# Performance work log

Hardware: AMD Instinct MI355X
Metric: run time of the kernel (lower is better)

## Reference

```python
import jax, jax.numpy as jnp
import numpy as np

TEMPERATURE = 12.5   # init temperature
SINKHORN_EPS = 0.05  # entropic regularization replacing exact cv2.EMD LP solve
SINKHORN_ITERS = 100 # fixed iteration count (jit-friendly)


def _weight_vector(A, B):
    # A: [M,C,H,W], B: [N,C,H,W] -> [M, N, H*W]
    # matches: global-avg-pool B over HW, inner product over channels per spatial node of A
    Bp = B.mean(axis=(2, 3))                      # [N, C]
    comb = jnp.einsum('mchw,nc->mnhw', A, Bp)     # [M, N, H, W]
    comb = comb.reshape(A.shape[0], B.shape[0], -1)
    return jax.nn.relu(comb) + 0.001


def _center(x):
    # norm='center': subtract channel mean (dim 1)
    return x - x.mean(axis=1, keepdims=True)


def _similarity_map(support, query):
    # metric='cosine': sim[q, w, i, j] = cos(query[q,:,i], support[w,:,j]) over channels
    s = support.reshape(support.shape[0], support.shape[1], -1)  # [W, C, Ns]
    q = query.reshape(query.shape[0], query.shape[1], -1)        # [Q, C, Nq]
    s = s / jnp.maximum(jnp.linalg.norm(s, axis=1, keepdims=True), 1e-8)
    q = q / jnp.maximum(jnp.linalg.norm(q, axis=1, keepdims=True), 1e-8)
    return jnp.einsum('qci,wcj->qwij', q, s)                     # [Q, W, Nq, Ns]


def _sinkhorn_flow(cost, a, b, eps=SINKHORN_EPS, n_iters=SINKHORN_ITERS):
    # Batched entropic OT in log-space. cost: [..., n, m]; a: [..., n]; b: [..., m].
    log_a = jnp.log(a)
    log_b = jnp.log(b)
    logK = -cost / eps

    def body(_, uv):
        u, v = uv
        u = log_a - jax.nn.logsumexp(logK + v[..., None, :], axis=-1)
        v = log_b - jax.nn.logsumexp(logK + u[..., None], axis=-2)
        return (u, v)

    u0 = jnp.zeros_like(log_a)
    v0 = jnp.zeros_like(log_b)
    u, v = jax.lax.fori_loop(0, n_iters, body, (u0, v0))
    return jnp.exp(logK + u[..., None] + v[..., None, :])  # transport plan [..., n, m]


def setup_inputs() -> dict:
    key = jax.random.key(0)
    k1, k2 = jax.random.split(key)
    support = jax.random.normal(k1, (32, 512, 8, 8), dtype=jnp.float32)
    query = jax.random.normal(k2, (256, 512, 8, 8), dtype=jnp.float32)
    return {"support": support, "query": query}


def reference(support, query):
    # weight_1: [Q, W, N] (row/query-node marginals), weight_2: [W, Q, N] (col/support-node)
    w1 = _weight_vector(query, support)
    w2 = _weight_vector(support, query)

    s = _center(support)
    q = _center(query)
    sim = _similarity_map(s, q)  # [Q, W, N, N]

    num_node = w1.shape[-1]
    # opencv path: relu (no-op, already >0) + 1e-5, rescale so each marginal sums to num_node
    a = w1 + 1e-5
    a = a * (num_node / a.sum(-1, keepdims=True))              # [Q, W, N]
    b = jnp.transpose(w2, (1, 0, 2)) + 1e-5                    # weight_2[j, i] -> [Q, W, N]
    b = b * (num_node / b.sum(-1, keepdims=True))

    flow = _sinkhorn_flow(1.0 - sim, a, b)                     # [Q, W, N, N]
    flow = jax.lax.stop_gradient(flow)  # opencv flow is a non-differentiable constant

    logits = (sim * flow).sum((-1, -2)) * (TEMPERATURE / num_node)  # [Q, W]
    return logits
```

## Files before the change

### kernel.cpp

```cpp
#include <hip/hip_runtime.h>
#include <math.h>


#define DEV static __device__ __forceinline__

typedef _Float16 half8 __attribute__((ext_vector_type(8)));
typedef float floatx4 __attribute__((ext_vector_type(4)));
typedef float floatx2 __attribute__((ext_vector_type(2)));

DEV float fast_rcp(float x) {
#if __has_builtin(__builtin_amdgcn_rcpf)
    return __builtin_amdgcn_rcpf(x);
#else
    return 1.0f / x;
#endif
}
DEV float fexp2(float x) {
#if __has_builtin(__builtin_amdgcn_exp2f)
    return __builtin_amdgcn_exp2f(x);
#else
    return exp2f(x);
#endif
}
DEV float flog2(float x) {
#if __has_builtin(__builtin_amdgcn_logf)
    return __builtin_amdgcn_logf(x);
#else
    return log2f(x);
#endif
}
DEV floatx2 pk_mul(floatx2 a, floatx2 b) {
    floatx2 d;
    asm("v_pk_mul_f32 %0, %1, %2" : "=v"(d) : "v"(a), "v"(b));
    return d;
}
DEV floatx2 pk_fma(floatx2 a, floatx2 b, floatx2 c) {
    floatx2 d;
    asm("v_pk_fma_f32 %0, %1, %2, %3" : "=v"(d) : "v"(a), "v"(b), "v"(c));
    return d;
}

#define K_SIM2M 28.853900817779268f
#define K_M2SIM 0.034657359027997264f
#define LDPH 72

__global__ void __launch_bounds__(1024, 1)
norm_kernel(const float* __restrict__ support, const float* __restrict__ query,
            _Float16* __restrict__ Vht, _Float16* __restrict__ Uht,
            float* __restrict__ muA, float* __restrict__ nrmA,
            float* __restrict__ Ssc) {
    __shared__ float red1[16][64];
    __shared__ float red2[16][64];
    __shared__ float muL[64], invL[64];
    __shared__ float tile[128][65];

    int sid = blockIdx.x;
    const float* src;
    _Float16* dst;
    if (sid < 32) {
        src = support + (size_t)sid * 32768; dst = Vht + (size_t)sid * 32768;
    } else {
        src = query + (size_t)(sid - 32) * 32768; dst = Uht + (size_t)(sid - 32) * 32768;
    }

    int node = threadIdx.x & 63;
    int cq   = threadIdx.x >> 6;

    float s1 = 0.f, s2 = 0.f;
#pragma unroll 8
    for (int j = 0; j < 32; ++j) {
        int c = cq * 32 + j;
        float x = src[c * 64 + node];
        s1 += x; s2 += x * x;
    }
    red1[cq][node] = s1;
    red2[cq][node] = s2;
    __syncthreads();
    if (threadIdx.x < 64) {
        float t1 = 0.f, t2 = 0.f;
#pragma unroll
        for (int k = 0; k < 16; ++k) { t1 += red1[k][node]; t2 += red2[k][node]; }
        float mu  = t1 * (1.0f / 512.0f);
        float ss  = t2 - 512.0f * mu * mu;
        float nrm = fmaxf(sqrtf(fmaxf(ss, 0.0f)), 1e-8f);
        muL[node]  = mu;
        invL[node] = 1.0f / nrm;
        muA[sid * 64 + node]  = mu;
        nrmA[sid * 64 + node] = nrm;
        float sS = t1;
        sS += __shfl_xor(sS, 1);  sS += __shfl_xor(sS, 2);  sS += __shfl_xor(sS, 4);
        sS += __shfl_xor(sS, 8);  sS += __shfl_xor(sS, 16); sS += __shfl_xor(sS, 32);
        if (node == 0) Ssc[sid] = sS * (1.0f / 64.0f);
    }
    __syncthreads();

    float mu = muL[node], inv = invL[node];
    for (int ch = 0; ch < 4; ++ch) {
#pragma unroll
        for (int j = 0; j < 8; ++j) {
            int cl = cq * 8 + j;
            float x = src[(ch * 128 + cl) * 64 + node];
            tile[cl][node] = (x - mu) * inv;
        }
        __syncthreads();
        {
            int g    = threadIdx.x;
            int slot = g & 63;
            int t    = (g >> 6) & 3;
            int kkl  = g >> 8;
            int nd   = t * 16 + (slot & 15);
            int c8   = (kkl << 2) | (slot >> 4);
            half8 v;
#pragma unroll
            for (int i = 0; i < 8; ++i) v[i] = (_Float16)tile[c8 * 8 + i][nd];
            *(half8*)(dst + ((size_t)ch * 1024 + g) * 8) = v;
        }
        __syncthreads();
    }
}

__global__ void __launch_bounds__(256, 4)
emd_kernel(const _Float16* __restrict__ Uht, const _Float16* __restrict__ Vht,
           const float* __restrict__ muA, const float* __restrict__ nrmA,
           const float* __restrict__ Ssc, float* __restrict__ out) {
    __shared__ __align__(16) _Float16 T[4][64 * LDPH];
    __shared__ float dAB[4][128];

    int x    = blockIdx.x & 7;
    int i    = blockIdx.x >> 3;
    int w    = i & 31;
    int wave = threadIdx.x >> 6;
    int lane = threadIdx.x & 63;
    int q    = x * 32 + (i >> 5) * 4 + wave;
    int lo16 = lane & 15;
    int hi4  = lane >> 4;
    int ig   = lane >> 3;
    int jg   = lane & 7;

    floatx4 acc[4][4];
#pragma unroll
    for (int tm = 0; tm < 4; ++tm)
#pragma unroll
        for (int tn = 0; tn < 4; ++tn)
            acc[tm][tn] = (floatx4){0.f, 0.f, 0.f, 0.f};

    const _Float16* Abase = Uht + (size_t)q * 32768 + lane * 8;
    const _Float16* Bbase = Vht + (size_t)w * 32768 + lane * 8;
#pragma unroll 1
    for (int kk = 0; kk < 16; ++kk) {
        half8 bf[4];
#pragma unroll
        for (int t = 0; t < 4; ++t)
            bf[t] = *(const half8*)(Bbase + (size_t)(kk * 4 + t) * 512);
#pragma unroll
        for (int tm = 0; tm < 4; ++tm) {
            half8 af = *(const half8*)(Abase + (size_t)(kk * 4 + tm) * 512);
#pragma unroll
            for (int tn = 0; tn < 4; ++tn)
                acc[tm][tn] = __builtin_amdgcn_mfma_f32_16x16x32_f16(
                    af, bf[tn], acc[tm][tn], 0, 0, 0);
        }
    }

    {
        float nw[4];
#pragma unroll
        for (int tn = 0; tn < 4; ++tn)
            nw[tn] = nrmA[w * 64 + tn * 16 + lo16];
        float4 nq[4];
#pragma unroll
        for (int tm = 0; tm < 4; ++tm)
            nq[tm] = *(const float4*)(nrmA + (32 + q) * 64 + tm * 16 + hi4 * 4);

        float pA[4][4];
#pragma unroll
        for (int tm = 0; tm < 4; ++tm)
#pragma unroll
            for (int r = 0; r < 4; ++r) {
                float s = acc[tm][0][r] * nw[0];
                s = fmaf(acc[tm][1][r], nw[1], s);
                s = fmaf(acc[tm][2][r], nw[2], s);
                s = fmaf(acc[tm][3][r], nw[3], s);
                s += __shfl_xor(s, 1); s += __shfl_xor(s, 2);
                s += __shfl_xor(s, 4); s += __shfl_xor(s, 8);
                pA[tm][r] = s;
            }
        float pB[4];
#pragma unroll
        for (int tn = 0; tn < 4; ++tn) {
            float s = acc[0][tn][0] * nq[0].x;
            s = fmaf(acc[0][tn][1], nq[0].y, s);
            s = fmaf(acc[0][tn][2], nq[0].z, s);
            s = fmaf(acc[0][tn][3], nq[0].w, s);
#pragma unroll
            for (int tm = 1; tm < 4; ++tm) {
                s = fmaf(acc[tm][tn][0], nq[tm].x, s);
                s = fmaf(acc[tm][tn][1], nq[tm].y, s);
                s = fmaf(acc[tm][tn][2], nq[tm].z, s);
                s = fmaf(acc[tm][tn][3], nq[tm].w, s);
            }
            s += __shfl_xor(s, 16); s += __shfl_xor(s, 32);
            pB[tn] = s;
        }
        float* dA = dAB[wave];
        float* dB = dAB[wave] + 64;
        if (lo16 == 0) {
#pragma unroll
            for (int tm = 0; tm < 4; ++tm)
#pragma unroll
                for (int r = 0; r < 4; ++r)
                    dA[tm * 16 + hi4 * 4 + r] = pA[tm][r] * 0.015625f;
        }
        if (hi4 == 0) {
#pragma unroll
            for (int tn = 0; tn < 4; ++tn)
                dB[tn * 16 + lo16] = pB[tn] * 0.015625f;
        }
    }

    float lmax = -2.0f;
#pragma unroll
    for (int tm = 0; tm < 4; ++tm)
#pragma unroll
        for (int tn = 0; tn < 4; ++tn)
#pragma unroll
            for (int r = 0; r < 4; ++r) lmax = fmaxf(lmax, acc[tm][tn][r]);
    lmax = fmaxf(lmax, __shfl_xor(lmax, 1));
    lmax = fmaxf(lmax, __shfl_xor(lmax, 2));
    lmax = fmaxf(lmax, __shfl_xor(lmax, 4));
    lmax = fmaxf(lmax, __shfl_xor(lmax, 8));
    lmax = fmaxf(lmax, __shfl_xor(lmax, 16));
    lmax = fmaxf(lmax, __shfl_xor(lmax, 32));
    float s0 = lmax;

    {
        _Float16* buf = T[wave];
#pragma unroll
        for (int tm = 0; tm < 4; ++tm)
#pragma unroll
            for (int tn = 0; tn < 4; ++tn)
#pragma unroll
                for (int r = 0; r < 4; ++r) {
                    int row = tm * 16 + hi4 * 4 + r;
                    int col = tn * 16 + lo16;
                    int sp  = (col & 7) ^ (row >> 3);
                    buf[row * LDPH + (col & ~7) + sp] =
                        (_Float16)fexp2((acc[tm][tn][r] - s0) * K_SIM2M);
                }
    }
    floatx2 Mp[8][4];
    {
        const _Float16* buf = T[wave];
#pragma unroll
        for (int t = 0; t < 8; ++t) {
            half8 h = *(const half8*)(buf + (ig * 8 + (jg ^ t)) * LDPH + jg * 8);
#pragma unroll
            for (int j = 0; j < 4; ++j)
                Mp[t][j] = (floatx2){(float)h[2 * j], (float)h[2 * j + 1]};
        }
    }

    int gp = q * 32 + w;
    float a_own, b_own;
    {
        const float* dA = dAB[wave];
        const float* dB = dAB[wave] + 64;
        float Sw = Ssc[w];
        float Sq = Ssc[32 + q];
        float muq = muA[(32 + q) * 64 + lane];
        float nrq = nrmA[(32 + q) * 64 + lane];
        float va = fmaxf(fmaf(muq, Sw, nrq * dA[lane]), 0.0f) + 0.001f;
        va += 1e-5f;
        float sa = va;
        sa += __shfl_xor(sa, 1);  sa += __shfl_xor(sa, 2);  sa += __shfl_xor(sa, 4);
        sa += __shfl_xor(sa, 8);  sa += __shfl_xor(sa, 16); sa += __shfl_xor(sa, 32);
        a_own = va * (64.0f / sa);
        int nb = ((lane & 7) << 3) | (lane >> 3);
        float muw = muA[w * 64 + nb];
        float nrw = nrmA[w * 64 + nb];
        float vb = fmaxf(fmaf(muw, Sq, nrw * dB[nb]), 0.0f) + 0.001f;
        vb += 1e-5f;
        float sb = vb;
        sb += __shfl_xor(sb, 1);  sb += __shfl_xor(sb, 2);  sb += __shfl_xor(sb, 4);
        sb += __shfl_xor(sb, 8);  sb += __shfl_xor(sb, 16); sb += __shfl_xor(sb, 32);
        b_own = vb * (64.0f / sb);
    }

    floatx2 wv2[4];
#pragma unroll
    for (int j = 0; j < 4; ++j) wv2[j] = (floatx2){1.f, 1.f};
    float q8[8];
    float w_prev = -1.f;

#pragma unroll 1
    for (int it = 0; it < 100; ++it) {
        float p[8];
#pragma unroll
        for (int t = 0; t < 8; ++t) {
            floatx2 s2 = pk_mul(Mp[t][0], wv2[0]);
            s2 = pk_fma(Mp[t][1], wv2[1], s2);
            s2 = pk_fma(Mp[t][2], wv2[2], s2);
            s2 = pk_fma(Mp[t][3], wv2[3], s2);
            p[t] = s2[0] + s2[1];
        }
        p[0] += __shfl_xor(p[4], 4); p[1] += __shfl_xor(p[5], 4);
        p[2] += __shfl_xor(p[6], 4); p[3] += __shfl_xor(p[7], 4);
        p[0] += __shfl_xor(p[2], 2); p[1] += __shfl_xor(p[3], 2);
        p[0] += __shfl_xor(p[1], 1);
        float z_own = a_own * fast_rcp(p[0]);
        q8[0] = z_own;
        q8[1] = __shfl_xor(q8[0], 1);
        q8[2] = __shfl_xor(q8[0], 2); q8[3] = __shfl_xor(q8[1], 2);
        q8[4] = __shfl_xor(q8[0], 4); q8[5] = __shfl_xor(q8[1], 4);
        q8[6] = __shfl_xor(q8[2], 4); q8[7] = __shfl_xor(q8[3], 4);
        floatx2 c2[4];
#pragma unroll
        for (int j = 0; j < 4; ++j) {
            floatx2 qb0 = (floatx2){q8[0], q8[0]};
            c2[j] = pk_mul(Mp[0][j], qb0);
        }
#pragma unroll
        for (int t = 1; t < 8; ++t) {
            floatx2 qb = (floatx2){q8[t], q8[t]};
#pragma unroll
            for (int j = 0; j < 4; ++j)
                c2[j] = pk_fma(Mp[t][j], qb, c2[j]);
        }
        float cp[8];
#pragma unroll
        for (int j = 0; j < 4; ++j) { cp[2 * j] = c2[j][0]; cp[2 * j + 1] = c2[j][1]; }
        cp[0] += __shfl_xor(cp[4], 32); cp[1] += __shfl_xor(cp[5], 32);
        cp[2] += __shfl_xor(cp[6], 32); cp[3] += __shfl_xor(cp[7], 32);
        cp[0] += __shfl_xor(cp[2], 16); cp[1] += __shfl_xor(cp[3], 16);
        cp[0] += __shfl_xor(cp[1], 8);
        float w_own = b_own * fast_rcp(cp[0]);
        float w8_0 = w_own;
        float w8_1 = __shfl_xor(w8_0, 8);
        float w8_2 = __shfl_xor(w8_0, 16), w8_3 = __shfl_xor(w8_1, 16);
        float w8_4 = __shfl_xor(w8_0, 32), w8_5 = __shfl_xor(w8_1, 32);
        float w8_6 = __shfl_xor(w8_2, 32), w8_7 = __shfl_xor(w8_3, 32);
        wv2[0] = (floatx2){w8_0, w8_1};
        wv2[1] = (floatx2){w8_2, w8_3};
        wv2[2] = (floatx2){w8_4, w8_5};
        wv2[3] = (floatx2){w8_6, w8_7};
        bool same = fabsf(w_own - w_prev) <= 1e-5f * w_own;
        w_prev = w_own;
        if (__all(same)) break;
    }

    float s = 0.f;
#pragma unroll
    for (int t = 0; t < 8; ++t)
#pragma unroll
        for (int c = 0; c < 8; ++c) {
            float m    = fmaxf(Mp[t][c >> 1][c & 1], 1e-30f);
            float sim  = fmaf(flog2(m), K_M2SIM, s0);
            float flow = q8[t] * m * wv2[c >> 1][c & 1];
            s = fmaf(sim, flow, s);
        }
    s += __shfl_xor(s, 1);  s += __shfl_xor(s, 2);  s += __shfl_xor(s, 4);
    s += __shfl_xor(s, 8);  s += __shfl_xor(s, 16); s += __shfl_xor(s, 32);
    if (lane == 0) out[gp] = s * 0.1953125f;
}

extern "C" void kernel_launch(void* const* d_in, const int* in_sizes, int n_in,
                              void* d_out, int out_size, void* d_ws, size_t ws_size,
                              hipStream_t stream) {
    (void)in_sizes; (void)n_in; (void)out_size; (void)ws_size;
    const float* support = (const float*)d_in[0];
    const float* query   = (const float*)d_in[1];

    char* ws = (char*)d_ws;
    _Float16* Uht  = (_Float16*)ws;
    _Float16* Vht  = Uht + 8388608;
    float* muA  = (float*)(Vht + 1048576);
    float* nrmA = muA + 18432;
    float* Ssc  = nrmA + 18432;

    norm_kernel<<<288, 1024, 0, stream>>>(support, query, Vht, Uht,
                                          muA, nrmA, Ssc);
    emd_kernel<<<2048, 256, 0, stream>>>(Uht, Vht, muA, nrmA, Ssc,
                                         (float*)d_out);
}
```

Before: 149.8 us.

## Split normalization kernel into stats and transpose kernels with vectorized loads

The single 288-block, 1024-thread normalization kernel becomes two launches. A stats kernel computes per-node mean and norm using float4 loads. A transpose kernel with 1152 blocks, one per sample and channel quarter, normalizes and converts to fp16 layout. The aim is more parallelism across CUs and wider memory accesses in the preprocessing stage. In exchange it adds an extra kernel launch and reads the input twice.

```diff
diff --git a/kernel.cpp b/kernel.cpp
--- a/kernel.cpp
+++ b/kernel.cpp
@@ -44,17 +44,57 @@
 #define K_M2SIM 0.034657359027997264f
 #define LDPH 72
 
-__global__ void __launch_bounds__(1024, 1)
-norm_kernel(const float* __restrict__ support, const float* __restrict__ query,
-            _Float16* __restrict__ Vht, _Float16* __restrict__ Uht,
-            float* __restrict__ muA, float* __restrict__ nrmA,
-            float* __restrict__ Ssc) {
+__global__ void __launch_bounds__(256)
+stats_kernel(const float* __restrict__ support, const float* __restrict__ query,
+             float* __restrict__ muA, float* __restrict__ nrmA,
+             float* __restrict__ Ssc) {
     __shared__ float red1[16][64];
     __shared__ float red2[16][64];
+
+    int sid = blockIdx.x;
+    const float* src = (sid < 32) ? support + (size_t)sid * 32768
+                                  : query + (size_t)(sid - 32) * 32768;
+    int ng = threadIdx.x & 15;
+    int cg = threadIdx.x >> 4;
+
+    float4 s1 = {0.f, 0.f, 0.f, 0.f}, s2 = {0.f, 0.f, 0.f, 0.f};
+    const float* base = src + ng * 4;
+#pragma unroll 8
+    for (int j = 0; j < 32; ++j) {
+        float4 v = *(const float4*)(base + (size_t)(cg * 32 + j) * 64);
+        s1.x += v.x; s1.y += v.y; s1.z += v.z; s1.w += v.w;
+        s2.x = fmaf(v.x, v.x, s2.x); s2.y = fmaf(v.y, v.y, s2.y);
+        s2.z = fmaf(v.z, v.z, s2.z); s2.w = fmaf(v.w, v.w, s2.w);
+    }
+    *(float4*)&red1[cg][ng * 4] = s1;
+    *(float4*)&red2[cg][ng * 4] = s2;
+    __syncthreads();
+    if (threadIdx.x < 64) {
+        int node = threadIdx.x;
+        float t1 = 0.f, t2 = 0.f;
+#pragma unroll
+        for (int k = 0; k < 16; ++k) { t1 += red1[k][node]; t2 += red2[k][node]; }
+        float mu  = t1 * (1.0f / 512.0f);
+        float ss  = t2 - 512.0f * mu * mu;
+        float nrm = fmaxf(sqrtf(fmaxf(ss, 0.0f)), 1e-8f);
+        muA[sid * 64 + node]  = mu;
+        nrmA[sid * 64 + node] = nrm;
+        float sS = t1;
+        sS += __shfl_xor(sS, 1);  sS += __shfl_xor(sS, 2);  sS += __shfl_xor(sS, 4);
+        sS += __shfl_xor(sS, 8);  sS += __shfl_xor(sS, 16); sS += __shfl_xor(sS, 32);
+        if (node == 0) Ssc[sid] = sS * (1.0f / 64.0f);
+    }
+}
+
+__global__ void __launch_bounds__(256)
+xpose_kernel(const float* __restrict__ support, const float* __restrict__ query,
+             const float* __restrict__ muA, const float* __restrict__ nrmA,
+             _Float16* __restrict__ Vht, _Float16* __restrict__ Uht) {
+    __shared__ float tile[128][65];
     __shared__ float muL[64], invL[64];
-    __shared__ float tile[128][65];
-
-    int sid = blockIdx.x;
+
+    int sid = blockIdx.x >> 2;
+    int ch  = blockIdx.x & 3;
     const float* src;
     _Float16* dst;
     if (sid < 32) {
@@ -62,60 +102,37 @@
     } else {
         src = query + (size_t)(sid - 32) * 32768; dst = Uht + (size_t)(sid - 32) * 32768;
     }
-
-    int node = threadIdx.x & 63;
-    int cq   = threadIdx.x >> 6;
-
-    float s1 = 0.f, s2 = 0.f;
-#pragma unroll 8
-    for (int j = 0; j < 32; ++j) {
-        int c = cq * 32 + j;
-        float x = src[c * 64 + node];
-        s1 += x; s2 += x * x;
-    }
-    red1[cq][node] = s1;
-    red2[cq][node] = s2;
+    if (threadIdx.x < 64) {
+        muL[threadIdx.x]  = muA[sid * 64 + threadIdx.x];
+        invL[threadIdx.x] = 1.0f / nrmA[sid * 64 + threadIdx.x];
+    }
     __syncthreads();
-    if (threadIdx.x < 64) {
-        float t1 = 0.f, t2 = 0.f;
-#pragma unroll
-        for (int k = 0; k < 16; ++k) { t1 += red1[k][node]; t2 += red2[k][node]; }
-        float mu  = t1 * (1.0f / 512.0f);
-        float ss  = t2 - 512.0f * mu * mu;
-        float nrm = fmaxf(sqrtf(fmaxf(ss, 0.0f)), 1e-8f);
-        muL[node]  = mu;
-        invL[node] = 1.0f / nrm;
-        muA[sid * 64 + node]  = mu;
-        nrmA[sid * 64 + node] = nrm;
-        float sS = t1;
-        sS += __shfl_xor(sS, 1);  sS += __shfl_xor(sS, 2);  sS += __shfl_xor(sS, 4);
-        sS += __shfl_xor(sS, 8);  sS += __shfl_xor(sS, 16); sS += __shfl_xor(sS, 32);
-        if (node == 0) Ssc[sid] = sS * (1.0f / 64.0f);
+
+#pragma unroll
+    for (int i = 0; i < 8; ++i) {
+        int f = i * 256 + threadIdx.x;
+        int c = f >> 4, k = f & 15;
+        float4 v = *(const float4*)(src + (size_t)(ch * 128 + c) * 64 + k * 4);
+        float4 m  = *(const float4*)&muL[k * 4];
+        float4 iv = *(const float4*)&invL[k * 4];
+        v.x = (v.x - m.x) * iv.x; v.y = (v.y - m.y) * iv.y;
+        v.z = (v.z - m.z) * iv.z; v.w = (v.w - m.w) * iv.w;
+        *(float4*)&tile[c][k * 4] = v;
     }
     __syncthreads();
 
-    float mu = muL[node], inv = invL[node];
-    for (int ch = 0; ch < 4; ++ch) {
-#pragma unroll
-        for (int j = 0; j < 8; ++j) {
-            int cl = cq * 8 + j;
-            float x = src[(ch * 128 + cl) * 64 + node];
-            tile[cl][node] = (x - mu) * inv;
-        }
-        __syncthreads();
-        {
-            int g    = threadIdx.x;
-            int slot = g & 63;
-            int t    = (g >> 6) & 3;
-            int kkl  = g >> 8;
-            int nd   = t * 16 + (slot & 15);
-            int c8   = (kkl << 2) | (slot >> 4);
-            half8 v;
-#pragma unroll
-            for (int i = 0; i < 8; ++i) v[i] = (_Float16)tile[c8 * 8 + i][nd];
-            *(half8*)(dst + ((size_t)ch * 1024 + g) * 8) = v;
-        }
-        __syncthreads();
+#pragma unroll
+    for (int i = 0; i < 4; ++i) {
+        int g    = i * 256 + threadIdx.x;
+        int slot = g & 63;
+        int tq   = (g >> 6) & 3;
+        int kkl  = g >> 8;
+        int nd   = tq * 16 + (slot & 15);
+        int c8   = (kkl << 2) | (slot >> 4);
+        half8 v;
+#pragma unroll
+        for (int jj = 0; jj < 8; ++jj) v[jj] = (_Float16)tile[c8 * 8 + jj][nd];
+        *(half8*)(dst + ((size_t)ch * 1024 + g) * 8) = v;
     }
 }
 
@@ -377,8 +394,8 @@
     float* nrmA = muA + 18432;
     float* Ssc  = nrmA + 18432;
 
-    norm_kernel<<<288, 1024, 0, stream>>>(support, query, Vht, Uht,
-                                          muA, nrmA, Ssc);
+    stats_kernel<<<288, 256, 0, stream>>>(support, query, muA, nrmA, Ssc);
+    xpose_kernel<<<1152, 256, 0, stream>>>(support, query, muA, nrmA, Vht, Uht);
     emd_kernel<<<2048, 256, 0, stream>>>(Uht, Vht, muA, nrmA, Ssc,
                                          (float*)d_out);
 }
```

New measurement: 152.3 us. About the same (+1.6%).
